# Kernel optimization log

Hardware: AMD Instinct MI355X
Metric: run time of the kernel (lower is better)

The kernel has to match this reference:

```python
import jax, jax.numpy as jnp
import numpy as np

VOCAB, X, H, C_CLS = 32000, 300, 512, 5
B, N_LEAVES = 256, 256  # complete binary trees, depth 9, 511 nodes/tree

def setup_inputs() -> dict:
    key = jax.random.key(0)
    ks = jax.random.split(key, 10)
    s = lambda k, shp, fan: jax.random.normal(k, shp, jnp.float32) * (1.0 / np.sqrt(fan))
    return {
        'wordid': jax.random.randint(ks[0], (B, N_LEAVES), 0, VOCAB),
        'emb': jax.random.normal(ks[1], (VOCAB, X), jnp.float32) * 0.1,
        'W_iou_w': s(ks[2], (3 * H, X), X),
        'W_iou_b': jnp.zeros((3 * H,), jnp.float32),
        'U_iou_w': s(ks[3], (3 * H, 2 * H), 2 * H),
        'U_iou_b': jnp.zeros((3 * H,), jnp.float32),
        'U_f_w': s(ks[4], (2 * H, 2 * H), 2 * H),
        'U_f_b': jnp.zeros((2 * H,), jnp.float32),
        'lin_w': s(ks[5], (C_CLS, H), H),
        'lin_b': jnp.zeros((C_CLS,), jnp.float32),
    }

def _cell(iou, c_f):
    i, o, u = jnp.split(iou, 3, axis=-1)
    c = jax.nn.sigmoid(i) * jnp.tanh(u) + c_f
    h = jax.nn.sigmoid(o) * jnp.tanh(c)
    return h, c

def reference(wordid, emb, W_iou_w, W_iou_b, U_iou_w, U_iou_b, U_f_w, U_f_b, lin_w, lin_b):
    b, n = wordid.shape
    # leaves: is_leaf=1 -> iou = W_iou(x), c_f = 0
    x = emb[wordid]                                   # [B, L, X]
    iou = x @ W_iou_w.T + W_iou_b                     # [B, L, 3H]
    h, c = _cell(iou, 0.0)
    hs = [h]
    # internal levels: reduce over exactly 2 children (binary TreeLSTM)
    while h.shape[1] > 1:
        m = h.shape[1] // 2
        h_cat = h.reshape(b, m, 2 * H)                # concat of 2 children
        c_pair = c.reshape(b, m, 2, H)
        f = jax.nn.sigmoid(h_cat @ U_f_w.T + U_f_b).reshape(b, m, 2, H)
        c_f = jnp.sum(f * c_pair, axis=2)             # [B, m, H]
        iou = h_cat @ U_iou_w.T + U_iou_b             # is_leaf=0 branch
        h, c = _cell(iou, c_f)
        hs.append(h)
    h_all = jnp.concatenate(hs, axis=1)               # [B, 2L-1, H], leaves-first topo order
    # dropout is identity at inference
    logits = h_all @ lin_w.T + lin_b                  # [B, 2L-1, num_classes]
    return logits
```

## Files before the change

kernel.cpp:

```cpp
#include <hip/hip_runtime.h>
#include <hip/hip_bf16.h>


typedef __bf16 bf16;
typedef bf16  bf16x8 __attribute__((ext_vector_type(8)));
typedef float f32x4  __attribute__((ext_vector_type(4)));

__device__ __forceinline__ float sigm(float x){ return 1.0f/(1.0f + __expf(-x)); }
__device__ __forceinline__ float tanh_f(float x){ return 1.0f - 2.0f/(__expf(2.0f*x)+1.0f); }

__global__ void cvt_all(const float* __restrict__ Wiou, const float* __restrict__ Uiou,
                        const float* __restrict__ Uf, const float* __restrict__ emb,
                        bf16* __restrict__ Wpad, bf16* __restrict__ Uall,
                        bf16* __restrict__ embp){
  const int b = blockIdx.x, t = threadIdx.x;
  if (b < 1536){
    Wpad[b*320 + t] = (bf16)(t < 300 ? Wiou[b*300 + t] : 0.f);
  } else if (b < 1536 + 32000){
    const int r = b - 1536;
    embp[(size_t)r*320 + t] = (bf16)(t < 300 ? emb[(size_t)r*300 + t] : 0.f);
  } else {
    const size_t i = (size_t)(b - 33536)*320 + t;
    if (i < (size_t)1536*1024) Uall[i] = (bf16)Uiou[i];
    else                       Uall[i] = (bf16)Uf[i - (size_t)1536*1024];
  }
}

__global__ __launch_bounds__(256, 2)
void leaf128_kernel(const int* __restrict__ wordid, const bf16* __restrict__ embp,
                    const bf16* __restrict__ Wpad, const float* __restrict__ Wb,
                    bf16* __restrict__ hcur, float* __restrict__ ccur)
{
  __shared__ bf16 lsA[128*40];
  __shared__ bf16 lsB[3][64*40];
  const int t = threadIdx.x;
  const int mrow0 = blockIdx.x*128, nblk = blockIdx.y*64;
  const int r = t>>2, kc = (t&3)*8;
  const int lane16 = t&15, quad = (t&63)>>4, w = t>>6;

  f32x4 acc[3][8];
  const f32x4 zero = {0.f,0.f,0.f,0.f};
  #pragma unroll
  for(int o=0;o<3;o++){
    #pragma unroll
    for(int rt=0;rt<8;rt++) acc[o][rt]=zero;
  }

  const int wid0 = wordid[mrow0 + r];
  const int wid1 = wordid[mrow0 + 64 + r];
  const bf16* arow0 = embp + (size_t)wid0*320;
  const bf16* arow1 = embp + (size_t)wid1*320;
  const int col = nblk + r;
  for (int k0=0;k0<320;k0+=32){
    *(bf16x8*)&lsA[r*40+kc]      = *(const bf16x8*)&arow0[k0+kc];
    *(bf16x8*)&lsA[(64+r)*40+kc] = *(const bf16x8*)&arow1[k0+kc];
    #pragma unroll
    for(int g=0;g<3;g++)
      *(bf16x8*)&lsB[g][r*40+kc] = *(const bf16x8*)&Wpad[(size_t)(g*512+col)*320 + k0+kc];
    __syncthreads();
    bf16x8 bfrag[3];
    #pragma unroll
    for(int g=0;g<3;g++) bfrag[g] = *(const bf16x8*)&lsB[g][(w*16+lane16)*40 + quad*8];
    #pragma unroll
    for(int rt=0;rt<8;rt++){
      bf16x8 a = *(const bf16x8*)&lsA[(rt*16+lane16)*40 + quad*8];
      #pragma unroll
      for(int g=0;g<3;g++)
        acc[g][rt] = __builtin_amdgcn_mfma_f32_16x16x32_bf16(a, bfrag[g], acc[g][rt], 0,0,0);
    }
    __syncthreads();
  }
  const int j = nblk + w*16 + lane16;
  const float bi=Wb[j], bo=Wb[512+j], bu=Wb[1024+j];
  #pragma unroll
  for(int rt=0;rt<8;rt++){
    #pragma unroll
    for(int reg=0;reg<4;reg++){
      const int row = mrow0 + rt*16 + quad*4 + reg;
      float iv=acc[0][rt][reg]+bi, ov=acc[1][rt][reg]+bo, uv=acc[2][rt][reg]+bu;
      float c = sigm(iv)*tanh_f(uv);
      float h = sigm(ov)*tanh_f(c);
      ccur[(size_t)row*512 + j] = c;
      hcur[(size_t)row*512 + j] = (bf16)h;
    }
  }
}

__global__ __launch_bounds__(256)
void level_kernel(const bf16* __restrict__ hprev, bf16* __restrict__ hcur,
                  const float* __restrict__ cprev, float* __restrict__ ccur,
                  const bf16* __restrict__ Uall, const float* __restrict__ Uioub,
                  const float* __restrict__ Ufb)
{
  __shared__ bf16 lsA[64*40];
  __shared__ bf16 lsB[5][64*40];
  const int t = threadIdx.x;
  const int mrow0 = blockIdx.x*64, nblk = blockIdx.y*64;
  const int r = t>>2, kc = (t&3)*8;
  const int lane16 = t&15, quad = (t&63)>>4, w = t>>6;

  f32x4 acc[5][4];
  const f32x4 zero = {0.f,0.f,0.f,0.f};
  #pragma unroll
  for(int o=0;o<5;o++){
    #pragma unroll
    for(int rt=0;rt<4;rt++) acc[o][rt]=zero;
  }

  const bf16* arow = hprev + (size_t)(mrow0 + r)*1024;
  const int col = nblk + r;
  for (int k0=0;k0<1024;k0+=32){
    *(bf16x8*)&lsA[r*40+kc] = *(const bf16x8*)&arow[k0+kc];
    #pragma unroll
    for(int g=0;g<5;g++)
      *(bf16x8*)&lsB[g][r*40+kc] = *(const bf16x8*)&Uall[(size_t)(g*512+col)*1024 + k0+kc];
    __syncthreads();
    bf16x8 bfrag[5];
    #pragma unroll
    for(int o=0;o<5;o++) bfrag[o] = *(const bf16x8*)&lsB[o][(w*16+lane16)*40 + quad*8];
    #pragma unroll
    for(int rt=0;rt<4;rt++){
      bf16x8 a = *(const bf16x8*)&lsA[(rt*16+lane16)*40 + quad*8];
      #pragma unroll
      for(int o=0;o<5;o++)
        acc[o][rt] = __builtin_amdgcn_mfma_f32_16x16x32_bf16(a, bfrag[o], acc[o][rt], 0,0,0);
    }
    __syncthreads();
  }
  const int j = nblk + w*16 + lane16;
  const float bi =Uioub[j], bo=Uioub[512+j], bu=Uioub[1024+j];
  const float bfl=Ufb[j],   bfr=Ufb[512+j];
  #pragma unroll
  for(int rt=0;rt<4;rt++){
    #pragma unroll
    for(int reg=0;reg<4;reg++){
      const int row = mrow0 + rt*16 + quad*4 + reg;
      float iv=acc[0][rt][reg]+bi, ov=acc[1][rt][reg]+bo, uv=acc[2][rt][reg]+bu;
      float fl=acc[3][rt][reg]+bfl, fr=acc[4][rt][reg]+bfr;
      float cl = cprev[((size_t)row*2  )*512 + j];
      float cr = cprev[((size_t)row*2+1)*512 + j];
      float cf = sigm(fl)*cl + sigm(fr)*cr;
      float c  = sigm(iv)*tanh_f(uv) + cf;
      float h  = sigm(ov)*tanh_f(c);
      ccur[(size_t)row*512 + j] = c;
      hcur[(size_t)row*512 + j] = (bf16)h;
    }
  }
}

__global__ __launch_bounds__(256, 2)
void level128_kernel(const bf16* __restrict__ hprev, bf16* __restrict__ hcur,
                     const float* __restrict__ cprev, float* __restrict__ ccur,
                     const bf16* __restrict__ Uall, const float* __restrict__ Uioub,
                     const float* __restrict__ Ufb)
{
  __shared__ bf16 lsA[128*40];
  __shared__ bf16 lsB[5][64*40];
  const int t = threadIdx.x;
  const int mrow0 = blockIdx.x*128, nblk = blockIdx.y*64;
  const int r = t>>2, kc = (t&3)*8;
  const int lane16 = t&15, quad = (t&63)>>4, w = t>>6;

  f32x4 acc[5][8];
  const f32x4 zero = {0.f,0.f,0.f,0.f};
  #pragma unroll
  for(int o=0;o<5;o++){
    #pragma unroll
    for(int rt=0;rt<8;rt++) acc[o][rt]=zero;
  }

  const bf16* arow0 = hprev + (size_t)(mrow0 + r)*1024;
  const bf16* arow1 = hprev + (size_t)(mrow0 + 64 + r)*1024;
  const int col = nblk + r;
  for (int k0=0;k0<1024;k0+=32){
    *(bf16x8*)&lsA[r*40+kc]      = *(const bf16x8*)&arow0[k0+kc];
    *(bf16x8*)&lsA[(64+r)*40+kc] = *(const bf16x8*)&arow1[k0+kc];
    #pragma unroll
    for(int g=0;g<5;g++)
      *(bf16x8*)&lsB[g][r*40+kc] = *(const bf16x8*)&Uall[(size_t)(g*512+col)*1024 + k0+kc];
    __syncthreads();
    bf16x8 bfrag[5];
    #pragma unroll
    for(int g=0;g<5;g++) bfrag[g] = *(const bf16x8*)&lsB[g][(w*16+lane16)*40 + quad*8];
    #pragma unroll
    for(int rt=0;rt<8;rt++){
      bf16x8 a = *(const bf16x8*)&lsA[(rt*16+lane16)*40 + quad*8];
      #pragma unroll
      for(int g=0;g<5;g++)
        acc[g][rt] = __builtin_amdgcn_mfma_f32_16x16x32_bf16(a, bfrag[g], acc[g][rt], 0,0,0);
    }
    __syncthreads();
  }
  const int j = nblk + w*16 + lane16;
  const float bi =Uioub[j], bo=Uioub[512+j], bu=Uioub[1024+j];
  const float bfl=Ufb[j],   bfr=Ufb[512+j];
  #pragma unroll
  for(int rt=0;rt<8;rt++){
    #pragma unroll
    for(int reg=0;reg<4;reg++){
      const int row = mrow0 + rt*16 + quad*4 + reg;
      float iv=acc[0][rt][reg]+bi, ov=acc[1][rt][reg]+bo, uv=acc[2][rt][reg]+bu;
      float fl=acc[3][rt][reg]+bfl, fr=acc[4][rt][reg]+bfr;
      float cl = cprev[((size_t)row*2  )*512 + j];
      float cr = cprev[((size_t)row*2+1)*512 + j];
      float cf = sigm(fl)*cl + sigm(fr)*cr;
      float c  = sigm(iv)*tanh_f(uv) + cf;
      float h  = sigm(ov)*tanh_f(c);
      ccur[(size_t)row*512 + j] = c;
      hcur[(size_t)row*512 + j] = (bf16)h;
    }
  }
}

__global__ __launch_bounds__(256)
void logits_kernel(const bf16* __restrict__ h, const float* __restrict__ linw,
                   const float* __restrict__ linb, float* __restrict__ out,
                   int rowbase, int lgm, int mask, int off){
  const int row = blockIdx.x*4 + (threadIdx.x>>6);
  const int l = threadIdx.x & 63;
  bf16x8 hv = *(const bf16x8*)(h + (size_t)row*512 + l*8);
  float hf[8];
  #pragma unroll
  for(int jj=0;jj<8;jj++) hf[jj] = (float)hv[jj];
  float s[5];
  #pragma unroll
  for(int c=0;c<5;c++){
    const f32x4 w0 = *(const f32x4*)(linw + c*512 + l*8);
    const f32x4 w1 = *(const f32x4*)(linw + c*512 + l*8 + 4);
    float a = 0.f;
    #pragma unroll
    for(int jj=0;jj<4;jj++) a += hf[jj]*w0[jj] + hf[4+jj]*w1[jj];
    s[c]=a;
  }
  #pragma unroll
  for(int o=32;o>0;o>>=1){
    #pragma unroll
    for(int c=0;c<5;c++) s[c] += __shfl_down(s[c], o, 64);
  }
  if (l==0){
    const int g = rowbase + row;
    const int node = (g>>lgm)*511 + off + (g&mask);
    #pragma unroll
    for(int c=0;c<5;c++) out[(size_t)node*5+c] = s[c] + linb[c];
  }
}

__global__ __launch_bounds__(256)
void logits2_kernel(const bf16* __restrict__ ha, int rows_a, int lgm_a, int mask_a, int off_a,
                    const bf16* __restrict__ hb, int lgm_b, int mask_b, int off_b,
                    const float* __restrict__ linw, const float* __restrict__ linb,
                    float* __restrict__ out){
  const int row = blockIdx.x*4 + (threadIdx.x>>6);
  const int l = threadIdx.x & 63;
  const bf16* hrow; int g, lgm, mask, off;
  if (row < rows_a){ hrow = ha + (size_t)row*512;            g = row;           lgm=lgm_a; mask=mask_a; off=off_a; }
  else             { hrow = hb + (size_t)(row-rows_a)*512;   g = row - rows_a;  lgm=lgm_b; mask=mask_b; off=off_b; }
  bf16x8 hv = *(const bf16x8*)(hrow + l*8);
  float hf[8];
  #pragma unroll
  for(int jj=0;jj<8;jj++) hf[jj] = (float)hv[jj];
  float s[5];
  #pragma unroll
  for(int c=0;c<5;c++){
    const f32x4 w0 = *(const f32x4*)(linw + c*512 + l*8);
    const f32x4 w1 = *(const f32x4*)(linw + c*512 + l*8 + 4);
    float a = 0.f;
    #pragma unroll
    for(int jj=0;jj<4;jj++) a += hf[jj]*w0[jj] + hf[4+jj]*w1[jj];
    s[c]=a;
  }
  #pragma unroll
  for(int o=32;o>0;o>>=1){
    #pragma unroll
    for(int c=0;c<5;c++) s[c] += __shfl_down(s[c], o, 64);
  }
  if (l==0){
    const int node = (g>>lgm)*511 + off + (g&mask);
    #pragma unroll
    for(int c=0;c<5;c++) out[(size_t)node*5+c] = s[c] + linb[c];
  }
}

__global__ void zero_out(float* out, int n){
  int i = blockIdx.x*256 + threadIdx.x;
  if (i < n) out[i] = 0.f;
}

extern "C" void kernel_launch(void* const* d_in, const int* in_sizes, int n_in,
                              void* d_out, int out_size, void* d_ws, size_t ws_size,
                              hipStream_t stream)
{
  const int*   wordid = (const int*)d_in[0];
  const float* emb    = (const float*)d_in[1];
  const float* Wiou   = (const float*)d_in[2];
  const float* Wioub  = (const float*)d_in[3];
  const float* Uiou   = (const float*)d_in[4];
  const float* Uioub  = (const float*)d_in[5];
  const float* Uf     = (const float*)d_in[6];
  const float* Ufb    = (const float*)d_in[7];
  const float* linw   = (const float*)d_in[8];
  const float* linb   = (const float*)d_in[9];
  float* out = (float*)d_out;

  const size_t oWPD  = 0;
  const size_t oUALL = oWPD  + (size_t)1536*320*2;
  const size_t oEMB  = oUALL + (size_t)2560*1024*2;
  const size_t oH1   = oEMB  + (size_t)32000*320*2;
  const size_t oC1   = oH1   + (size_t)32768*512*2;
  const size_t oH0   = oC1   + (size_t)32768*512*4;
  size_t R0 = 0;
  {
    const size_t t2 = oH0 + (size_t)32768*512*(2+4);
    const size_t t4 = oH0 + (size_t)16384*512*(2+4);
    const size_t t8 = oH0 + (size_t) 8192*512*(2+4);
    if      (ws_size >= t2) R0 = 32768;
    else if (ws_size >= t4) R0 = 16384;
    else if (ws_size >= t8) R0 = 8192;
  }
  if (R0 == 0){
    zero_out<<<(out_size+255)/256, 256, 0, stream>>>(out, out_size);
    return;
  }

  char* ws = (char*)d_ws;
  bf16*  Wpad = (bf16*)(ws + oWPD);
  bf16*  Uall = (bf16*)(ws + oUALL);
  bf16*  embp = (bf16*)(ws + oEMB);
  bf16*  h1   = (bf16*)(ws + oH1);
  float* c1   = (float*)(ws + oC1);
  bf16*  h0   = (bf16*)(ws + oH0);
  float* c0   = (float*)(ws + oH0 + R0*1024);

  cvt_all<<<41728, 320, 0, stream>>>(Wiou, Uiou, Uf, emb, Wpad, Uall, embp);

  const int offs[9] = {0,256,384,448,480,496,504,508,510};
  const int nchunk = (int)(65536 / R0);

  for (int ch = 0; ch < nchunk; ch++){
    const int* wid = wordid + (size_t)ch*R0;
    leaf128_kernel<<<dim3((int)(R0/128), 8), 256, 0, stream>>>(wid, embp, Wpad, Wioub,
                                                               h0, c0);
    logits_kernel<<<(int)(R0/4), 256, 0, stream>>>(h0, linw, linb, out,
                                                   (int)(ch*R0), 8, 255, 0);
    bf16*  h1c = h1 + (size_t)ch*(R0/2)*512;
    float* c1c = c1 + (size_t)ch*(R0/2)*512;
    const int orows = (int)(R0/2);
    level128_kernel<<<dim3(orows/128, 8), 256, 0, stream>>>(h0, h1c, c0, c1c,
                                                            Uall, Uioub, Ufb);
  }

  for (int lv = 2; lv <= 8; lv++){
    const int rows = 65536 >> lv;
    const bf16*  hin  = (lv & 1) ? h0 : h1;
    bf16*        hout = (lv & 1) ? h1 : h0;
    const float* cin  = (lv & 1) ? c0 : c1;
    float*       cout = (lv & 1) ? c1 : c0;
    if (rows >= 4096)
      level128_kernel<<<dim3(rows/128, 8), 256, 0, stream>>>(hin, hout, cin, cout,
                                                             Uall, Uioub, Ufb);
    else
      level_kernel<<<dim3(rows/64, 8), 256, 0, stream>>>(hin, hout, cin, cout,
                                                         Uall, Uioub, Ufb);
    if ((lv & 1) == 0){
      const int rows_a = 65536 >> (lv-1);
      const int rows_b = rows;
      logits2_kernel<<<(rows_a + rows_b)/4, 256, 0, stream>>>(
          h1, rows_a, 8-(lv-1), (256>>(lv-1))-1, offs[lv-1],
          h0,         8-lv,     (256>>lv)-1,     offs[lv],
          linw, linb, out);
    }
  }
}
```

Measured before the change: 859.4 us.

## Double-buffer GEMM tiles with direct global-to-LDS loads and XOR swizzle

Replaces the register-staged global-to-shared copies in the leaf and 128-row level kernels with direct global_load_lds transfers into double-buffered LDS tiles. The next K-slice is prefetched while the MFMA loop runs on the current one, and one barrier per iteration is dropped. The padded row stride (40) gives way to an XOR-swizzled 32-wide layout to avoid bank conflicts. This doubles LDS use per block, which may reduce occupancy, and correctness depends on the swizzle mapping matching the wave-uniform LDS destination semantics of global_load_lds.

```diff
diff --git a/kernel.cpp b/kernel.cpp
--- a/kernel.cpp
+++ b/kernel.cpp
@@ -8,6 +8,12 @@
 
 __device__ __forceinline__ float sigm(float x){ return 1.0f/(1.0f + __expf(-x)); }
 __device__ __forceinline__ float tanh_f(float x){ return 1.0f - 2.0f/(__expf(2.0f*x)+1.0f); }
+
+__device__ __forceinline__ void gload16(const bf16* g, bf16* l){
+  __builtin_amdgcn_global_load_lds(
+      (const __attribute__((address_space(1))) void*)g,
+      (__attribute__((address_space(3))) void*)l, 16, 0, 0);
+}
 
 __global__ void cvt_all(const float* __restrict__ Wiou, const float* __restrict__ Uiou,
                         const float* __restrict__ Uf, const float* __restrict__ emb,
@@ -31,12 +37,27 @@
                     const bf16* __restrict__ Wpad, const float* __restrict__ Wb,
                     bf16* __restrict__ hcur, float* __restrict__ ccur)
 {
-  __shared__ bf16 lsA[128*40];
-  __shared__ bf16 lsB[3][64*40];
+  __shared__ bf16 lsA[2][128*32];
+  __shared__ bf16 lsB[2][192*32];
   const int t = threadIdx.x;
   const int mrow0 = blockIdx.x*128, nblk = blockIdx.y*64;
-  const int r = t>>2, kc = (t&3)*8;
   const int lane16 = t&15, quad = (t&63)>>4, w = t>>6;
+
+  const int lrow = t>>2;
+  const int qsw  = ((t&3) ^ ((t>>3)&3))*8;
+  const int wb   = (t & 192)*8;
+
+  const int wid0 = wordid[mrow0 + lrow];
+  const int wid1 = wordid[mrow0 + 64 + lrow];
+  const bf16* srcA0 = embp + (size_t)wid0*320 + qsw;
+  const bf16* srcA1 = embp + (size_t)wid1*320 + qsw;
+  const bf16* srcB0 = Wpad + (size_t)(0*512 + nblk + lrow)*320 + qsw;
+  const bf16* srcB1 = Wpad + (size_t)(1*512 + nblk + lrow)*320 + qsw;
+  const bf16* srcB2 = Wpad + (size_t)(2*512 + nblk + lrow)*320 + qsw;
+
+  const int sA   = (t>>1)&3;
+  const int aoff = lane16*32 + ((quad ^ sA)*8);
+  const int boff = (w*16 + lane16)*32 + ((quad ^ sA)*8);
 
   f32x4 acc[3][8];
   const f32x4 zero = {0.f,0.f,0.f,0.f};
@@ -46,29 +67,38 @@
     for(int rt=0;rt<8;rt++) acc[o][rt]=zero;
   }
 
-  const int wid0 = wordid[mrow0 + r];
-  const int wid1 = wordid[mrow0 + 64 + r];
-  const bf16* arow0 = embp + (size_t)wid0*320;
-  const bf16* arow1 = embp + (size_t)wid1*320;
-  const int col = nblk + r;
-  for (int k0=0;k0<320;k0+=32){
-    *(bf16x8*)&lsA[r*40+kc]      = *(const bf16x8*)&arow0[k0+kc];
-    *(bf16x8*)&lsA[(64+r)*40+kc] = *(const bf16x8*)&arow1[k0+kc];
-    #pragma unroll
-    for(int g=0;g<3;g++)
-      *(bf16x8*)&lsB[g][r*40+kc] = *(const bf16x8*)&Wpad[(size_t)(g*512+col)*320 + k0+kc];
-    __syncthreads();
+  {
+    bf16* dA = lsA[0]; bf16* dB = lsB[0];
+    gload16(srcA0, dA + wb);
+    gload16(srcA1, dA + 2048 + wb);
+    gload16(srcB0, dB + wb);
+    gload16(srcB1, dB + 2048 + wb);
+    gload16(srcB2, dB + 4096 + wb);
+  }
+  __syncthreads();
+  int cur = 0;
+  for (int ks = 0; ks < 10; ks++){
+    if (ks < 9){
+      const int k0 = (ks+1)*32;
+      bf16* dA = lsA[cur^1]; bf16* dB = lsB[cur^1];
+      gload16(srcA0 + k0, dA + wb);
+      gload16(srcA1 + k0, dA + 2048 + wb);
+      gload16(srcB0 + k0, dB + wb);
+      gload16(srcB1 + k0, dB + 2048 + wb);
+      gload16(srcB2 + k0, dB + 4096 + wb);
+    }
     bf16x8 bfrag[3];
     #pragma unroll
-    for(int g=0;g<3;g++) bfrag[g] = *(const bf16x8*)&lsB[g][(w*16+lane16)*40 + quad*8];
+    for(int g=0;g<3;g++) bfrag[g] = *(const bf16x8*)&lsB[cur][g*2048 + boff];
     #pragma unroll
     for(int rt=0;rt<8;rt++){
-      bf16x8 a = *(const bf16x8*)&lsA[(rt*16+lane16)*40 + quad*8];
+      bf16x8 a = *(const bf16x8*)&lsA[cur][rt*512 + aoff];
       #pragma unroll
       for(int g=0;g<3;g++)
         acc[g][rt] = __builtin_amdgcn_mfma_f32_16x16x32_bf16(a, bfrag[g], acc[g][rt], 0,0,0);
     }
     __syncthreads();
+    cur ^= 1;
   }
   const int j = nblk + w*16 + lane16;
   const float bi=Wb[j], bo=Wb[512+j], bu=Wb[1024+j];
@@ -154,12 +184,27 @@
                      const bf16* __restrict__ Uall, const float* __restrict__ Uioub,
                      const float* __restrict__ Ufb)
 {
-  __shared__ bf16 lsA[128*40];
-  __shared__ bf16 lsB[5][64*40];
+  __shared__ bf16 lsA[2][128*32];
+  __shared__ bf16 lsB[2][320*32];
   const int t = threadIdx.x;
   const int mrow0 = blockIdx.x*128, nblk = blockIdx.y*64;
-  const int r = t>>2, kc = (t&3)*8;
   const int lane16 = t&15, quad = (t&63)>>4, w = t>>6;
+
+  const int lrow = t>>2;
+  const int qsw  = ((t&3) ^ ((t>>3)&3))*8;
+  const int wb   = (t & 192)*8;
+
+  const bf16* srcA0 = hprev + (size_t)(mrow0 + lrow)*1024 + qsw;
+  const bf16* srcA1 = hprev + (size_t)(mrow0 + 64 + lrow)*1024 + qsw;
+  const bf16* srcB0 = Uall + (size_t)(0*512 + nblk + lrow)*1024 + qsw;
+  const bf16* srcB1 = Uall + (size_t)(1*512 + nblk + lrow)*1024 + qsw;
+  const bf16* srcB2 = Uall + (size_t)(2*512 + nblk + lrow)*1024 + qsw;
+  const bf16* srcB3 = Uall + (size_t)(3*512 + nblk + lrow)*1024 + qsw;
+  const bf16* srcB4 = Uall + (size_t)(4*512 + nblk + lrow)*1024 + qsw;
+
+  const int sA   = (t>>1)&3;
+  const int aoff = lane16*32 + ((quad ^ sA)*8);
+  const int boff = (w*16 + lane16)*32 + ((quad ^ sA)*8);
 
   f32x4 acc[5][8];
   const f32x4 zero = {0.f,0.f,0.f,0.f};
@@ -169,27 +214,42 @@
     for(int rt=0;rt<8;rt++) acc[o][rt]=zero;
   }
 
-  const bf16* arow0 = hprev + (size_t)(mrow0 + r)*1024;
-  const bf16* arow1 = hprev + (size_t)(mrow0 + 64 + r)*1024;
-  const int col = nblk + r;
-  for (int k0=0;k0<1024;k0+=32){
-    *(bf16x8*)&lsA[r*40+kc]      = *(const bf16x8*)&arow0[k0+kc];
-    *(bf16x8*)&lsA[(64+r)*40+kc] = *(const bf16x8*)&arow1[k0+kc];
-    #pragma unroll
-    for(int g=0;g<5;g++)
-      *(bf16x8*)&lsB[g][r*40+kc] = *(const bf16x8*)&Uall[(size_t)(g*512+col)*1024 + k0+kc];
-    __syncthreads();
+  {
+    bf16* dA = lsA[0]; bf16* dB = lsB[0];
+    gload16(srcA0, dA + wb);
+    gload16(srcA1, dA + 2048 + wb);
+    gload16(srcB0, dB + wb);
+    gload16(srcB1, dB + 2048 + wb);
+    gload16(srcB2, dB + 4096 + wb);
+    gload16(srcB3, dB + 6144 + wb);
+    gload16(srcB4, dB + 8192 + wb);
+  }
+  __syncthreads();
+  int cur = 0;
+  for (int ks = 0; ks < 32; ks++){
+    if (ks < 31){
+      const int k0 = (ks+1)*32;
+      bf16* dA = lsA[cur^1]; bf16* dB = lsB[cur^1];
+      gload16(srcA0 + k0, dA + wb);
+      gload16(srcA1 + k0, dA + 2048 + wb);
+      gload16(srcB0 + k0, dB + wb);
+      gload16(srcB1 + k0, dB + 2048 + wb);
+      gload16(srcB2 + k0, dB + 4096 + wb);
+      gload16(srcB3 + k0, dB + 6144 + wb);
+      gload16(srcB4 + k0, dB + 8192 + wb);
+    }
     bf16x8 bfrag[5];
     #pragma unroll
-    for(int g=0;g<5;g++) bfrag[g] = *(const bf16x8*)&lsB[g][(w*16+lane16)*40 + quad*8];
+    for(int g=0;g<5;g++) bfrag[g] = *(const bf16x8*)&lsB[cur][g*2048 + boff];
     #pragma unroll
     for(int rt=0;rt<8;rt++){
-      bf16x8 a = *(const bf16x8*)&lsA[(rt*16+lane16)*40 + quad*8];
+      bf16x8 a = *(const bf16x8*)&lsA[cur][rt*512 + aoff];
       #pragma unroll
       for(int g=0;g<5;g++)
         acc[g][rt] = __builtin_amdgcn_mfma_f32_16x16x32_bf16(a, bfrag[g], acc[g][rt], 0,0,0);
     }
     __syncthreads();
+    cur ^= 1;
   }
   const int j = nblk + w*16 + lane16;
   const float bi =Uioub[j], bo=Uioub[512+j], bu=Uioub[1024+j];
```

New measurement: 865.2 us. No clear change (+0.7%).
